# Kernel optimization log

Measured on AMD Instinct MI355X. Metric: run time of the kernel, lower is better.

Reference implementation:

```python
import jax, jax.numpy as jnp
import numpy as np

N, H, W_SP, CIN = 32, 56, 56, 256
COUT, KH, KW = 256, 3, 3


def setup_inputs() -> dict:
    key = jax.random.key(0)
    k1, k2, k3 = jax.random.split(key, 3)
    x = jax.random.normal(k1, (N, H, W_SP, CIN), dtype=jnp.float32)
    W = jax.random.normal(k2, (KH, KW, CIN, COUT), dtype=jnp.float32) * 0.05
    b = jax.random.normal(k3, (COUT,), dtype=jnp.float32) * 0.05
    return {"x": x, "W": W, "b": b}


def reference(x, W, b):
    # Binarize weights to {-1, +1} via sign with straight-through estimator
    # (forward = sign(W), gradient = identity), matching tensorlayer's
    # binary_weight quantizer.
    bW = W + jax.lax.stop_gradient(jnp.sign(W) - W)
    # tf.nn.conv2d(x, bW, strides=(1,1,1,1), padding='SAME'), NHWC / HWIO
    y = jax.lax.conv_general_dilated(
        x, bW,
        window_strides=(1, 1),
        padding='SAME',
        dimension_numbers=('NHWC', 'HWIO', 'NHWC'),
    )
    y = y + b  # tf.nn.bias_add over channels
    return jax.nn.relu(y)
```

## Files before the change

### kernel.cpp

```cpp
#include <hip/hip_runtime.h>
#include <hip/hip_bf16.h>

#define CIN   256
#define COUT  256
#define HH    56
#define WW    56
#define NB    32
#define KTOT  2304
#define MTOT  (NB * HH * WW)

#define BM 128
#define BN 256
#define BK 32
#define NTHREADS 256
#define NSTEPS (KTOT / BK)

#define BT_BYTES  ((size_t)COUT * KTOT * 2)
#define XB_OFF    BT_BYTES
#define XB_BYTES  ((size_t)MTOT * CIN * 2)
#define ZB_OFF    (XB_OFF + XB_BYTES)
#define WS_NEEDED (ZB_OFF + 64)

typedef __attribute__((ext_vector_type(4))) float  f32x4;
typedef __attribute__((ext_vector_type(8))) __bf16 bf16x8;

__device__ __forceinline__ void gload_lds16(const void* g, void* l) {
    __builtin_amdgcn_global_load_lds(
        (const __attribute__((address_space(1))) void*)g,
        (__attribute__((address_space(3))) void*)l,
        16, 0, 0);
}

__global__ void xcast_kernel(const float* __restrict__ x, __bf16* __restrict__ xb,
                             float* __restrict__ zbuf) {
    const size_t total = (size_t)MTOT * CIN / 8;
    size_t idx = (size_t)blockIdx.x * blockDim.x + threadIdx.x;
    const size_t stride = (size_t)gridDim.x * blockDim.x;
    for (size_t g = idx; g < total; g += stride) {
        f32x4 v0 = ((const f32x4*)x)[2 * g];
        f32x4 v1 = ((const f32x4*)x)[2 * g + 1];
        bf16x8 o;
        o[0] = (__bf16)v0[0]; o[1] = (__bf16)v0[1];
        o[2] = (__bf16)v0[2]; o[3] = (__bf16)v0[3];
        o[4] = (__bf16)v1[0]; o[5] = (__bf16)v1[1];
        o[6] = (__bf16)v1[2]; o[7] = (__bf16)v1[3];
        ((bf16x8*)xb)[g] = o;
    }
    if (blockIdx.x == 0 && threadIdx.x < 16) zbuf[threadIdx.x] = 0.f;
}

__global__ void binarize_w_kernel(const float* __restrict__ W,
                                  unsigned short* __restrict__ bt) {
    int k  = blockIdx.x;
    int co = threadIdx.x;
    int tap = k >> 8, cin = k & 255;
    int c2 = cin >> 5, ci = cin & 31;
    int ks = c2 * 9 + tap;
    float w = W[(size_t)k * COUT + co];
    unsigned short s = (w > 0.f) ? 0x3F80u : ((w < 0.f) ? 0xBF80u : 0u);
    bt[(size_t)co * KTOT + ks * 32 + (ci ^ (((co >> 1) & 3) << 3))] = s;
}

__global__ __launch_bounds__(NTHREADS, 2)
void bconv_kernel(const __bf16* __restrict__ xb,
                  const unsigned short* __restrict__ bt,
                  const float* __restrict__ bias,
                  float* __restrict__ out,
                  const char* __restrict__ zb) {
    __shared__ __bf16 Al[2][BM][BK];
    __shared__ __bf16 Bl[2][BN][BK];

    const int tid  = threadIdx.x;
    const int lane = tid & 63;
    const int wid  = tid >> 6;

    const int bid = blockIdx.x;
    const int swz = (bid & 7) * (MTOT / BM / 8) + (bid >> 3);
    const int m_base = swz * BM;

    const int wn = wid * 64;

    long bBase[4];
#pragma unroll
    for (int j = 0; j < 4; ++j) {
        int co = j * 64 + wid * 16 + (lane >> 2);
        bBase[j] = (long)co * (KTOT * 2) + (long)(lane & 3) * 16;
    }

    const int schunk = (lane & 3) ^ ((lane >> 3) & 3);
    int aH[2], aW[2];
    long aBase[2];
#pragma unroll
    for (int i = 0; i < 2; ++i) {
        int r = wid * 32 + i * 16 + (lane >> 2);
        int flat = m_base + r;
        aW[i] = flat % WW;
        aH[i] = (flat / WW) % HH;
        aBase[i] = (long)flat * (CIN * 2) + schunk * 16;
    }

    f32x4 acc[8][4];
#pragma unroll
    for (int i = 0; i < 8; ++i)
#pragma unroll
        for (int j = 0; j < 4; ++j)
            acc[i][j] = (f32x4){0.f, 0.f, 0.f, 0.f};

    const char* xbb = (const char*)xb;
    const char* btb = (const char*)bt;

    auto STAGE = [&](int ks, int buf) {
#pragma unroll
        for (int j = 0; j < 4; ++j)
            gload_lds16(btb + bBase[j] + (long)ks * 64,
                        &Bl[buf][j * 64 + wid * 16][0]);
        const int c2  = ks / 9;
        const int tap = ks - c2 * 9;
        const int dh  = tap / 3 - 1;
        const int dw  = tap % 3 - 1;
        const long doff = (long)(dh * WW + dw) * (CIN * 2);
#pragma unroll
        for (int i = 0; i < 2; ++i) {
            int ih = aH[i] + dh, iw = aW[i] + dw;
            bool valid = ((unsigned)ih < (unsigned)HH) && ((unsigned)iw < (unsigned)WW);
            const char* g = valid ? (xbb + aBase[i] + doff + c2 * 64)
                                  : (const char*)zb;
            gload_lds16(g, &Al[buf][wid * 32 + i * 16][0]);
        }
    };

    STAGE(0, 0);

    const int rsel = lane & 15;
    const int cbyte = ((lane >> 4) ^ ((rsel >> 1) & 3)) * 16;

    for (int ks = 0; ks < NSTEPS; ++ks) {
        const int cur = ks & 1;
        if (ks + 1 < NSTEPS) {
            STAGE(ks + 1, cur ^ 1);
            asm volatile("s_waitcnt vmcnt(6)" ::: "memory");
        } else {
            asm volatile("s_waitcnt vmcnt(0)" ::: "memory");
        }
        __builtin_amdgcn_s_barrier();
        asm volatile("" ::: "memory");

        const char* Ab = (const char*)&Al[cur][0][0];
        const char* Bb = (const char*)&Bl[cur][0][0];
        bf16x8 af[8], bfr[4];
#pragma unroll
        for (int ni = 0; ni < 4; ++ni)
            bfr[ni] = *(const bf16x8*)(Bb + (wn + ni * 16 + rsel) * (BK * 2) + cbyte);
#pragma unroll
        for (int mi = 0; mi < 8; ++mi)
            af[mi] = *(const bf16x8*)(Ab + (mi * 16 + rsel) * (BK * 2) + cbyte);

        __builtin_amdgcn_s_setprio(1);
#pragma unroll
        for (int mi = 0; mi < 8; ++mi)
#pragma unroll
            for (int ni = 0; ni < 4; ++ni)
                acc[mi][ni] = __builtin_amdgcn_mfma_f32_16x16x32_bf16(
                    af[mi], bfr[ni], acc[mi][ni], 0, 0, 0);
        __builtin_amdgcn_s_setprio(0);

        asm volatile("s_waitcnt lgkmcnt(0)" ::: "memory");
        __builtin_amdgcn_s_barrier();
        asm volatile("" ::: "memory");
    }

    const int col_l  = lane & 15;
    const int row_g4 = (lane >> 4) * 4;
#pragma unroll
    for (int ni = 0; ni < 4; ++ni) {
        const int cout = wn + ni * 16 + col_l;
        const float bv = bias[cout];
#pragma unroll
        for (int mi = 0; mi < 8; ++mi) {
            const int row = m_base + mi * 16 + row_g4;
#pragma unroll
            for (int j = 0; j < 4; ++j) {
                float v = acc[mi][ni][j] + bv;
                out[(size_t)(row + j) * COUT + cout] = v > 0.f ? v : 0.f;
            }
        }
    }
}

__global__ void binarize_w_old_kernel(const float* __restrict__ W,
                                      unsigned short* __restrict__ bt) {
    int k  = blockIdx.x;
    int co = threadIdx.x;
    int tap = k >> 8, cin = k & 255;
    int c = cin >> 6, ci = cin & 63;
    int ks = c * 9 + tap;
    float w = W[(size_t)k * COUT + co];
    unsigned short s = (w > 0.f) ? 0x3F80u : ((w < 0.f) ? 0xBF80u : 0u);
    bt[(size_t)co * KTOT + ks * 64 + (ci ^ ((co & 7) << 3))] = s;
}

__global__ __launch_bounds__(512, 4)
void bconv_old_kernel(const float* __restrict__ x,
                      const unsigned short* __restrict__ bt,
                      const float* __restrict__ bias,
                      float* __restrict__ out) {
    __shared__ __bf16 Al[128][64];
    __shared__ __bf16 Bl[256][64];

    const int tid  = threadIdx.x;
    const int lane = tid & 63;
    const int wid  = tid >> 6;

    const int bid = blockIdx.x;
    const int swz = (bid & 7) * (MTOT / 128 / 8) + (bid >> 3);
    const int m_base = swz * 128;

    const int wm = (wid & 1) * 64;
    const int wn = (wid >> 1) * 64;

    const int  rB0 = wid * 32 + (lane >> 3);
    const long bB0 = (long)rB0 * (KTOT * 2) + (lane & 7) * 16;

    int aH[2], aW[2], aOff[2];
#pragma unroll
    for (int i = 0; i < 2; ++i) {
        int r = i * 64 + (tid >> 3);
        int flat = m_base + r;
        aW[i] = flat % WW;
        aH[i] = (flat / WW) % HH;
        aOff[i] = flat * (CIN * 4);
    }

    f32x4 acc[4][4];
#pragma unroll
    for (int i = 0; i < 4; ++i)
#pragma unroll
        for (int j = 0; j < 4; ++j)
            acc[i][j] = (f32x4){0.f, 0.f, 0.f, 0.f};

    const char* xfb = (const char*)x;
    const char* btb = (const char*)bt;

    for (int ks = 0; ks < 36; ++ks) {
        const int c    = ks / 9;
        const int tap  = ks % 9;
        const int dh   = tap / 3 - 1;
        const int dw   = tap % 3 - 1;
        const int doff = dh * WW + dw;

        __syncthreads();

#pragma unroll
        for (int i = 0; i < 4; ++i) {
            const char* g = btb + bB0 + (long)i * 8 * (KTOT * 2) + ks * 128;
            gload_lds16(g, &Bl[wid * 32 + i * 8][0]);
        }

        const int cg = tid & 7;
#pragma unroll
        for (int i = 0; i < 2; ++i) {
            int ih = aH[i] + dh, iw = aW[i] + dw;
            f32x4 v0 = (f32x4){0.f, 0.f, 0.f, 0.f};
            f32x4 v1 = (f32x4){0.f, 0.f, 0.f, 0.f};
            if (((unsigned)ih < (unsigned)HH) && ((unsigned)iw < (unsigned)WW)) {
                const float* gp = (const float*)(xfb +
                    (long)(aOff[i] + doff * (CIN * 4) + c * 256 + cg * 32));
                v0 = ((const f32x4*)gp)[0];
                v1 = ((const f32x4*)gp)[1];
            }
            bf16x8 o;
            o[0] = (__bf16)v0[0]; o[1] = (__bf16)v0[1];
            o[2] = (__bf16)v0[2]; o[3] = (__bf16)v0[3];
            o[4] = (__bf16)v1[0]; o[5] = (__bf16)v1[1];
            o[6] = (__bf16)v1[2]; o[7] = (__bf16)v1[3];
            int r = i * 64 + (tid >> 3);
            *(bf16x8*)((char*)&Al[0][0] + r * 128 + ((cg * 16) ^ ((r & 7) << 4))) = o;
        }

        __syncthreads();

        const char* Ab = (const char*)&Al[0][0];
        const char* Bb = (const char*)&Bl[0][0];
        const int swzr = (lane & 7) << 4;
        const int rsel = lane & 15;
        const int csel = (lane >> 4) * 16;
#pragma unroll
        for (int kk = 0; kk < 2; ++kk) {
            const int colb = kk * 64 + csel;
            bf16x8 af[4], bfr[4];
#pragma unroll
            for (int mi = 0; mi < 4; ++mi)
                af[mi] = *(const bf16x8*)(Ab + (wm + mi * 16 + rsel) * 128 + (colb ^ swzr));
#pragma unroll
            for (int ni = 0; ni < 4; ++ni)
                bfr[ni] = *(const bf16x8*)(Bb + (wn + ni * 16 + rsel) * 128 + (colb ^ swzr));
#pragma unroll
            for (int mi = 0; mi < 4; ++mi)
#pragma unroll
                for (int ni = 0; ni < 4; ++ni)
                    acc[mi][ni] = __builtin_amdgcn_mfma_f32_16x16x32_bf16(
                        af[mi], bfr[ni], acc[mi][ni], 0, 0, 0);
        }
    }

    const int col_l  = lane & 15;
    const int row_g4 = (lane >> 4) * 4;
#pragma unroll
    for (int ni = 0; ni < 4; ++ni) {
        const int cout = wn + ni * 16 + col_l;
        const float bv = bias[cout];
#pragma unroll
        for (int mi = 0; mi < 4; ++mi) {
            const int row = m_base + wm + mi * 16 + row_g4;
#pragma unroll
            for (int j = 0; j < 4; ++j) {
                float v = acc[mi][ni][j] + bv;
                out[(size_t)(row + j) * COUT + cout] = v > 0.f ? v : 0.f;
            }
        }
    }
}

extern "C" void kernel_launch(void* const* d_in, const int* in_sizes, int n_in,
                              void* d_out, int out_size, void* d_ws, size_t ws_size,
                              hipStream_t stream) {
    const float* x = (const float*)d_in[0];
    const float* W = (const float*)d_in[1];
    const float* b = (const float*)d_in[2];
    float* out = (float*)d_out;

    char* ws = (char*)d_ws;
    unsigned short* bt = (unsigned short*)ws;
    __bf16* xb   = (__bf16*)(ws + XB_OFF);
    float*  zbuf = (float*)(ws + ZB_OFF);

    if (ws_size >= WS_NEEDED) {
        binarize_w_kernel<<<dim3(KTOT), dim3(COUT), 0, stream>>>(W, bt);
        xcast_kernel<<<dim3(2048), dim3(256), 0, stream>>>(x, xb, zbuf);
        bconv_kernel<<<dim3(MTOT / BM), dim3(NTHREADS), 0, stream>>>(
            xb, bt, b, out, (const char*)zbuf);
    } else {
        binarize_w_old_kernel<<<dim3(KTOT), dim3(COUT), 0, stream>>>(W, bt);
        bconv_old_kernel<<<dim3(MTOT / 128), dim3(512), 0, stream>>>(x, bt, b, out);
    }
}
```

Measured before the change: 182.4 us.

## Use 8-wave blocks with 2x4 warp tiling and triple-buffered LDS prefetch

The block grows from 4 to 8 waves arranged as a 2x4 grid, so each wave computes a 64x64 sub-tile instead of 128x64. This halves per-wave accumulators and fragment loads, and each thread issues fewer global-to-LDS loads per stage. The single double buffer becomes a three-slot LDS ring that prefetches two K-steps ahead, with vmcnt waits adjusted to match, to hide more global load latency. The new launch bound of 4 blocks of 512 threads may squeeze the register budget and cause spills, and the larger LDS footprint limits how many blocks fit on a CU.

```diff
diff --git a/kernel.cpp b/kernel.cpp
--- a/kernel.cpp
+++ b/kernel.cpp
@@ -12,8 +12,9 @@
 #define BM 128
 #define BN 256
 #define BK 32
-#define NTHREADS 256
+#define NTHREADS 512
 #define NSTEPS (KTOT / BK)
+#define SLOT_ELEMS (BM * BK + BN * BK)
 
 #define BT_BYTES  ((size_t)COUT * KTOT * 2)
 #define XB_OFF    BT_BYTES
@@ -61,14 +62,13 @@
     bt[(size_t)co * KTOT + ks * 32 + (ci ^ (((co >> 1) & 3) << 3))] = s;
 }
 
-__global__ __launch_bounds__(NTHREADS, 2)
+__global__ __launch_bounds__(NTHREADS, 4)
 void bconv_kernel(const __bf16* __restrict__ xb,
                   const unsigned short* __restrict__ bt,
                   const float* __restrict__ bias,
                   float* __restrict__ out,
                   const char* __restrict__ zb) {
-    __shared__ __bf16 Al[2][BM][BK];
-    __shared__ __bf16 Bl[2][BN][BK];
+    __shared__ __bf16 lds[3 * SLOT_ELEMS];
 
     const int tid  = threadIdx.x;
     const int lane = tid & 63;
@@ -78,30 +78,30 @@
     const int swz = (bid & 7) * (MTOT / BM / 8) + (bid >> 3);
     const int m_base = swz * BM;
 
-    const int wn = wid * 64;
-
-    long bBase[4];
-#pragma unroll
-    for (int j = 0; j < 4; ++j) {
-        int co = j * 64 + wid * 16 + (lane >> 2);
-        bBase[j] = (long)co * (KTOT * 2) + (long)(lane & 3) * 16;
-    }
-
-    const int schunk = (lane & 3) ^ ((lane >> 3) & 3);
-    int aH[2], aW[2];
-    long aBase[2];
-#pragma unroll
-    for (int i = 0; i < 2; ++i) {
-        int r = wid * 32 + i * 16 + (lane >> 2);
+    const int wm = (wid >> 2) * 64;
+    const int wn = (wid & 3) * 64;
+
+    long bSrc[2];
+#pragma unroll
+    for (int j = 0; j < 2; ++j) {
+        int co = j * 128 + (tid >> 2);
+        bSrc[j] = (long)co * (KTOT * 2) + (long)(tid & 3) * 16;
+    }
+
+    const int schunk = (tid & 3) ^ ((tid >> 3) & 3);
+    int aHH, aWW;
+    long aBase;
+    {
+        int r = tid >> 2;
         int flat = m_base + r;
-        aW[i] = flat % WW;
-        aH[i] = (flat / WW) % HH;
-        aBase[i] = (long)flat * (CIN * 2) + schunk * 16;
-    }
-
-    f32x4 acc[8][4];
-#pragma unroll
-    for (int i = 0; i < 8; ++i)
+        aWW = flat % WW;
+        aHH = (flat / WW) % HH;
+        aBase = (long)flat * (CIN * 2) + schunk * 16;
+    }
+
+    f32x4 acc[4][4];
+#pragma unroll
+    for (int i = 0; i < 4; ++i)
 #pragma unroll
         for (int j = 0; j < 4; ++j)
             acc[i][j] = (f32x4){0.f, 0.f, 0.f, 0.f};
@@ -109,55 +109,59 @@
     const char* xbb = (const char*)xb;
     const char* btb = (const char*)bt;
 
-    auto STAGE = [&](int ks, int buf) {
-#pragma unroll
-        for (int j = 0; j < 4; ++j)
-            gload_lds16(btb + bBase[j] + (long)ks * 64,
-                        &Bl[buf][j * 64 + wid * 16][0]);
+    auto STAGE = [&](int ks, int slot) {
+        __bf16* As = &lds[slot * SLOT_ELEMS];
+        __bf16* Bs = As + BM * BK;
+#pragma unroll
+        for (int j = 0; j < 2; ++j)
+            gload_lds16(btb + bSrc[j] + (long)ks * 64,
+                        &Bs[(j * 128 + wid * 16) * BK]);
         const int c2  = ks / 9;
         const int tap = ks - c2 * 9;
         const int dh  = tap / 3 - 1;
         const int dw  = tap % 3 - 1;
-        const long doff = (long)(dh * WW + dw) * (CIN * 2);
-#pragma unroll
-        for (int i = 0; i < 2; ++i) {
-            int ih = aH[i] + dh, iw = aW[i] + dw;
-            bool valid = ((unsigned)ih < (unsigned)HH) && ((unsigned)iw < (unsigned)WW);
-            const char* g = valid ? (xbb + aBase[i] + doff + c2 * 64)
-                                  : (const char*)zb;
-            gload_lds16(g, &Al[buf][wid * 32 + i * 16][0]);
-        }
+        int ih = aHH + dh, iw = aWW + dw;
+        bool valid = ((unsigned)ih < (unsigned)HH) && ((unsigned)iw < (unsigned)WW);
+        const char* g = valid
+            ? (xbb + aBase + (long)(dh * WW + dw) * (CIN * 2) + c2 * 64)
+            : (const char*)zb;
+        gload_lds16(g, &As[(wid * 16) * BK]);
     };
 
     STAGE(0, 0);
-
-    const int rsel = lane & 15;
+    STAGE(1, 1);
+
+    const int rsel  = lane & 15;
     const int cbyte = ((lane >> 4) ^ ((rsel >> 1) & 3)) * 16;
 
-    for (int ks = 0; ks < NSTEPS; ++ks) {
-        const int cur = ks & 1;
-        if (ks + 1 < NSTEPS) {
-            STAGE(ks + 1, cur ^ 1);
+    int sc = 0;
+    for (int t = 0; t < NSTEPS; ++t) {
+        if (t < NSTEPS - 2) {
+            const int sp = (sc >= 1) ? (sc - 1) : 2;
+            STAGE(t + 2, sp);
             asm volatile("s_waitcnt vmcnt(6)" ::: "memory");
+        } else if (t == NSTEPS - 2) {
+            asm volatile("s_waitcnt vmcnt(3)" ::: "memory");
         } else {
             asm volatile("s_waitcnt vmcnt(0)" ::: "memory");
         }
         __builtin_amdgcn_s_barrier();
         asm volatile("" ::: "memory");
 
-        const char* Ab = (const char*)&Al[cur][0][0];
-        const char* Bb = (const char*)&Bl[cur][0][0];
-        bf16x8 af[8], bfr[4];
+        const char* As = (const char*)&lds[sc * SLOT_ELEMS];
+        const char* Bs = As + BM * BK * 2;
+
+        bf16x8 af[4], bfr[4];
+#pragma unroll
+        for (int mi = 0; mi < 4; ++mi)
+            af[mi] = *(const bf16x8*)(As + (wm + mi * 16 + rsel) * (BK * 2) + cbyte);
 #pragma unroll
         for (int ni = 0; ni < 4; ++ni)
-            bfr[ni] = *(const bf16x8*)(Bb + (wn + ni * 16 + rsel) * (BK * 2) + cbyte);
-#pragma unroll
-        for (int mi = 0; mi < 8; ++mi)
-            af[mi] = *(const bf16x8*)(Ab + (mi * 16 + rsel) * (BK * 2) + cbyte);
+            bfr[ni] = *(const bf16x8*)(Bs + (wn + ni * 16 + rsel) * (BK * 2) + cbyte);
 
         __builtin_amdgcn_s_setprio(1);
 #pragma unroll
-        for (int mi = 0; mi < 8; ++mi)
+        for (int mi = 0; mi < 4; ++mi)
 #pragma unroll
             for (int ni = 0; ni < 4; ++ni)
                 acc[mi][ni] = __builtin_amdgcn_mfma_f32_16x16x32_bf16(
@@ -167,6 +171,8 @@
         asm volatile("s_waitcnt lgkmcnt(0)" ::: "memory");
         __builtin_amdgcn_s_barrier();
         asm volatile("" ::: "memory");
+
+        sc = (sc < 2) ? (sc + 1) : 0;
     }
 
     const int col_l  = lane & 15;
@@ -176,8 +182,8 @@
         const int cout = wn + ni * 16 + col_l;
         const float bv = bias[cout];
 #pragma unroll
-        for (int mi = 0; mi < 8; ++mi) {
-            const int row = m_base + mi * 16 + row_g4;
+        for (int mi = 0; mi < 4; ++mi) {
+            const int row = m_base + wm + mi * 16 + row_g4;
 #pragma unroll
             for (int j = 0; j < 4; ++j) {
                 float v = acc[mi][ni][j] + bv;
```

Measured after the change: 157.5 us. 13.6% less time.

## Retile bconv to 256x128 blocks with 2x2 warp grid and N split

Applied to the files above, without the earlier changes.

Changes the block tile from 128x256 (M x N) to 256x128. The grid now splits the output channels in two, and the 4 waves are arranged as a 2x2 grid with 128x64 per-wave tiles. A unified LDS buffer replaces the separate A/B arrays, and launch bounds are raised to 3 blocks per CU to increase occupancy. The x tile is now fetched once per N-half, which doubles activation traffic. In exchange the grid is doubled and occupancy is higher, while the per-wave MFMA work and LDS footprint stay the same.

```diff
diff --git a/kernel.cpp b/kernel.cpp
--- a/kernel.cpp
+++ b/kernel.cpp
@@ -9,11 +9,12 @@
 #define KTOT  2304
 #define MTOT  (NB * HH * WW)
 
-#define BM 128
-#define BN 256
+#define BM 256
+#define BN 128
 #define BK 32
 #define NTHREADS 256
 #define NSTEPS (KTOT / BK)
+#define SLOT_ELEMS ((BM + BN) * BK)
 
 #define BT_BYTES  ((size_t)COUT * KTOT * 2)
 #define XB_OFF    BT_BYTES
@@ -61,38 +62,39 @@
     bt[(size_t)co * KTOT + ks * 32 + (ci ^ (((co >> 1) & 3) << 3))] = s;
 }
 
-__global__ __launch_bounds__(NTHREADS, 2)
+__global__ __launch_bounds__(NTHREADS, 3)
 void bconv_kernel(const __bf16* __restrict__ xb,
                   const unsigned short* __restrict__ bt,
                   const float* __restrict__ bias,
                   float* __restrict__ out,
                   const char* __restrict__ zb) {
-    __shared__ __bf16 Al[2][BM][BK];
-    __shared__ __bf16 Bl[2][BN][BK];
+    __shared__ __bf16 lds[2 * SLOT_ELEMS];
 
     const int tid  = threadIdx.x;
     const int lane = tid & 63;
     const int wid  = tid >> 6;
 
     const int bid = blockIdx.x;
-    const int swz = (bid & 7) * (MTOT / BM / 8) + (bid >> 3);
-    const int m_base = swz * BM;
-
-    const int wn = wid * 64;
-
-    long bBase[4];
-#pragma unroll
-    for (int j = 0; j < 4; ++j) {
-        int co = j * 64 + wid * 16 + (lane >> 2);
-        bBase[j] = (long)co * (KTOT * 2) + (long)(lane & 3) * 16;
-    }
-
-    const int schunk = (lane & 3) ^ ((lane >> 3) & 3);
-    int aH[2], aW[2];
-    long aBase[2];
-#pragma unroll
-    for (int i = 0; i < 2; ++i) {
-        int r = wid * 32 + i * 16 + (lane >> 2);
+    const int swz = (bid & 7) * 98 + (bid >> 3);
+    const int m_base = (swz >> 1) * BM;
+    const int n_base = (swz & 1) * BN;
+
+    const int wm = (wid >> 1) * 128;
+    const int wn = (wid & 1) * 64;
+
+    long bSrc[2];
+#pragma unroll
+    for (int j = 0; j < 2; ++j) {
+        int co = n_base + j * 64 + (tid >> 2);
+        bSrc[j] = (long)co * (KTOT * 2) + (long)(tid & 3) * 16;
+    }
+
+    const int schunk = (tid & 3) ^ ((tid >> 3) & 3);
+    int aH[4], aW[4];
+    long aBase[4];
+#pragma unroll
+    for (int i = 0; i < 4; ++i) {
+        int r = i * 64 + (tid >> 2);
         int flat = m_base + r;
         aW[i] = flat % WW;
         aH[i] = (flat / WW) % HH;
@@ -109,35 +111,36 @@
     const char* xbb = (const char*)xb;
     const char* btb = (const char*)bt;
 
-    auto STAGE = [&](int ks, int buf) {
-#pragma unroll
-        for (int j = 0; j < 4; ++j)
-            gload_lds16(btb + bBase[j] + (long)ks * 64,
-                        &Bl[buf][j * 64 + wid * 16][0]);
+    auto STAGE = [&](int ks, int slot) {
+        __bf16* As = &lds[slot * SLOT_ELEMS];
+        __bf16* Bs = As + BM * BK;
+#pragma unroll
+        for (int j = 0; j < 2; ++j)
+            gload_lds16(btb + bSrc[j] + (long)ks * 64,
+                        &Bs[(j * 64 + wid * 16) * BK]);
         const int c2  = ks / 9;
         const int tap = ks - c2 * 9;
         const int dh  = tap / 3 - 1;
         const int dw  = tap % 3 - 1;
-        const long doff = (long)(dh * WW + dw) * (CIN * 2);
-#pragma unroll
-        for (int i = 0; i < 2; ++i) {
+        const long soff = (long)(dh * WW + dw) * (CIN * 2) + c2 * 64;
+#pragma unroll
+        for (int i = 0; i < 4; ++i) {
             int ih = aH[i] + dh, iw = aW[i] + dw;
             bool valid = ((unsigned)ih < (unsigned)HH) && ((unsigned)iw < (unsigned)WW);
-            const char* g = valid ? (xbb + aBase[i] + doff + c2 * 64)
-                                  : (const char*)zb;
-            gload_lds16(g, &Al[buf][wid * 32 + i * 16][0]);
+            const char* g = valid ? (xbb + aBase[i] + soff) : (const char*)zb;
+            gload_lds16(g, &As[(i * 64 + wid * 16) * BK]);
         }
     };
 
     STAGE(0, 0);
 
-    const int rsel = lane & 15;
+    const int rsel  = lane & 15;
     const int cbyte = ((lane >> 4) ^ ((rsel >> 1) & 3)) * 16;
 
-    for (int ks = 0; ks < NSTEPS; ++ks) {
-        const int cur = ks & 1;
-        if (ks + 1 < NSTEPS) {
-            STAGE(ks + 1, cur ^ 1);
+    for (int t = 0; t < NSTEPS; ++t) {
+        const int cur = t & 1;
+        if (t + 1 < NSTEPS) {
+            STAGE(t + 1, cur ^ 1);
             asm volatile("s_waitcnt vmcnt(6)" ::: "memory");
         } else {
             asm volatile("s_waitcnt vmcnt(0)" ::: "memory");
@@ -145,15 +148,16 @@
         __builtin_amdgcn_s_barrier();
         asm volatile("" ::: "memory");
 
-        const char* Ab = (const char*)&Al[cur][0][0];
-        const char* Bb = (const char*)&Bl[cur][0][0];
+        const char* As = (const char*)&lds[cur * SLOT_ELEMS];
+        const char* Bs = As + BM * BK * 2;
+
         bf16x8 af[8], bfr[4];
 #pragma unroll
         for (int ni = 0; ni < 4; ++ni)
-            bfr[ni] = *(const bf16x8*)(Bb + (wn + ni * 16 + rsel) * (BK * 2) + cbyte);
+            bfr[ni] = *(const bf16x8*)(Bs + (wn + ni * 16 + rsel) * (BK * 2) + cbyte);
 #pragma unroll
         for (int mi = 0; mi < 8; ++mi)
-            af[mi] = *(const bf16x8*)(Ab + (mi * 16 + rsel) * (BK * 2) + cbyte);
+            af[mi] = *(const bf16x8*)(As + (wm + mi * 16 + rsel) * (BK * 2) + cbyte);
 
         __builtin_amdgcn_s_setprio(1);
 #pragma unroll
@@ -173,11 +177,11 @@
     const int row_g4 = (lane >> 4) * 4;
 #pragma unroll
     for (int ni = 0; ni < 4; ++ni) {
-        const int cout = wn + ni * 16 + col_l;
+        const int cout = n_base + wn + ni * 16 + col_l;
         const float bv = bias[cout];
 #pragma unroll
         for (int mi = 0; mi < 8; ++mi) {
-            const int row = m_base + mi * 16 + row_g4;
+            const int row = m_base + wm + mi * 16 + row_g4;
 #pragma unroll
             for (int j = 0; j < 4; ++j) {
                 float v = acc[mi][ni][j] + bv;
@@ -337,7 +341,7 @@
     if (ws_size >= WS_NEEDED) {
         binarize_w_kernel<<<dim3(KTOT), dim3(COUT), 0, stream>>>(W, bt);
         xcast_kernel<<<dim3(2048), dim3(256), 0, stream>>>(x, xb, zbuf);
-        bconv_kernel<<<dim3(MTOT / BM), dim3(NTHREADS), 0, stream>>>(
+        bconv_kernel<<<dim3((MTOT / BM) * (COUT / BN)), dim3(NTHREADS), 0, stream>>>(
             xb, bt, b, out, (const char*)zbuf);
     } else {
         binarize_w_old_kernel<<<dim3(KTOT), dim3(COUT), 0, stream>>>(W, bt);
```

After: 680.8 us. +273.3%, slower.

## Enlarge conv GEMM tile to 256x256 with split-K-half interleaved LDS pipeline

Applied to the files above, without the earlier changes.

Doubles the M tile to 256 rows and the thread count to 512, arranging 8 waves as a 2x4 grid. Each 64-wide K step is split into two 32-wide halves held in separate LDS regions, and the global-to-LDS loads for the next halves are issued between MFMA phases. This raises operand reuse per LDS byte and hides load latency under compute. The cost is a 128KB LDS footprint, which allows only one block per CU, and a grid with a partial last wave of blocks.

```diff
diff --git a/kernel.cpp b/kernel.cpp
--- a/kernel.cpp
+++ b/kernel.cpp
@@ -9,11 +9,11 @@
 #define KTOT  2304
 #define MTOT  (NB * HH * WW)
 
-#define BM 128
+#define BM 256
 #define BN 256
-#define BK 32
-#define NTHREADS 256
-#define NSTEPS (KTOT / BK)
+#define NTHREADS 512
+#define NT 36
+#define REG_ELEMS (256 * 32)
 
 #define BT_BYTES  ((size_t)COUT * KTOT * 2)
 #define XB_OFF    BT_BYTES
@@ -67,37 +67,34 @@
                   const float* __restrict__ bias,
                   float* __restrict__ out,
                   const char* __restrict__ zb) {
-    __shared__ __bf16 Al[2][BM][BK];
-    __shared__ __bf16 Bl[2][BN][BK];
+    __shared__ __bf16 lds[2][4][REG_ELEMS];
 
     const int tid  = threadIdx.x;
     const int lane = tid & 63;
     const int wid  = tid >> 6;
 
     const int bid = blockIdx.x;
-    const int swz = (bid & 7) * (MTOT / BM / 8) + (bid >> 3);
+    const int swz = (bid & 7) * 49 + (bid >> 3);
     const int m_base = swz * BM;
 
-    const int wn = wid * 64;
-
-    long bBase[4];
-#pragma unroll
-    for (int j = 0; j < 4; ++j) {
-        int co = j * 64 + wid * 16 + (lane >> 2);
-        bBase[j] = (long)co * (KTOT * 2) + (long)(lane & 3) * 16;
-    }
-
-    const int schunk = (lane & 3) ^ ((lane >> 3) & 3);
+    const int wm = (wid >> 2) * 128;
+    const int wn = (wid & 3) * 64;
+
+    const int schunk = (tid & 3) ^ ((tid >> 3) & 3);
     int aH[2], aW[2];
     long aBase[2];
 #pragma unroll
-    for (int i = 0; i < 2; ++i) {
-        int r = wid * 32 + i * 16 + (lane >> 2);
+    for (int j = 0; j < 2; ++j) {
+        int r = j * 128 + (tid >> 2);
         int flat = m_base + r;
-        aW[i] = flat % WW;
-        aH[i] = (flat / WW) % HH;
-        aBase[i] = (long)flat * (CIN * 2) + schunk * 16;
-    }
+        aW[j] = flat % WW;
+        aH[j] = (flat / WW) % HH;
+        aBase[j] = (long)flat * (CIN * 2) + schunk * 16;
+    }
+    long bBase[2];
+#pragma unroll
+    for (int j = 0; j < 2; ++j)
+        bBase[j] = (long)(j * 128 + (tid >> 2)) * (KTOT * 2) + (long)(tid & 3) * 16;
 
     f32x4 acc[8][4];
 #pragma unroll
@@ -109,64 +106,84 @@
     const char* xbb = (const char*)xb;
     const char* btb = (const char*)bt;
 
-    auto STAGE = [&](int ks, int buf) {
-#pragma unroll
-        for (int j = 0; j < 4; ++j)
-            gload_lds16(btb + bBase[j] + (long)ks * 64,
-                        &Bl[buf][j * 64 + wid * 16][0]);
-        const int c2  = ks / 9;
-        const int tap = ks - c2 * 9;
+    auto STAGE_A = [&](int ks, int h, int buf) {
+        const int c   = ks / 9;
+        const int tap = ks - c * 9;
         const int dh  = tap / 3 - 1;
         const int dw  = tap % 3 - 1;
-        const long doff = (long)(dh * WW + dw) * (CIN * 2);
-#pragma unroll
-        for (int i = 0; i < 2; ++i) {
-            int ih = aH[i] + dh, iw = aW[i] + dw;
+        const long soff = (long)(dh * WW + dw) * (CIN * 2) + c * 128 + h * 64;
+#pragma unroll
+        for (int j = 0; j < 2; ++j) {
+            int ih = aH[j] + dh, iw = aW[j] + dw;
             bool valid = ((unsigned)ih < (unsigned)HH) && ((unsigned)iw < (unsigned)WW);
-            const char* g = valid ? (xbb + aBase[i] + doff + c2 * 64)
-                                  : (const char*)zb;
-            gload_lds16(g, &Al[buf][wid * 32 + i * 16][0]);
+            const char* g = valid ? (xbb + aBase[j] + soff) : (const char*)zb;
+            gload_lds16(g, (char*)&lds[buf][h][0] + j * 8192 + wid * 1024);
         }
     };
-
-    STAGE(0, 0);
-
-    const int rsel = lane & 15;
+    auto STAGE_B = [&](int ks, int h, int buf) {
+        const int c   = ks / 9;
+        const int tap = ks - c * 9;
+        const long soff = (long)(((2 * c + h) * 9 + tap)) * 64;
+#pragma unroll
+        for (int j = 0; j < 2; ++j)
+            gload_lds16(btb + bBase[j] + soff,
+                        (char*)&lds[buf][2 + h][0] + j * 8192 + wid * 1024);
+    };
+
+    STAGE_A(0, 0, 0); STAGE_B(0, 0, 0);
+    STAGE_A(0, 1, 0); STAGE_B(0, 1, 0);
+    STAGE_A(1, 0, 1); STAGE_B(1, 0, 1);
+
+    const int rsel  = lane & 15;
     const int cbyte = ((lane >> 4) ^ ((rsel >> 1) & 3)) * 16;
 
-    for (int ks = 0; ks < NSTEPS; ++ks) {
-        const int cur = ks & 1;
-        if (ks + 1 < NSTEPS) {
-            STAGE(ks + 1, cur ^ 1);
-            asm volatile("s_waitcnt vmcnt(6)" ::: "memory");
-        } else {
-            asm volatile("s_waitcnt vmcnt(0)" ::: "memory");
-        }
+    bf16x8 bfr[4];
+    auto PH = [&](const char* Ar, const char* Br, int mf0, bool readB) {
+        if (readB) {
+#pragma unroll
+            for (int ni = 0; ni < 4; ++ni)
+                bfr[ni] = *(const bf16x8*)(Br + (wn + ni * 16 + rsel) * 64 + cbyte);
+        }
+        bf16x8 af[4];
+#pragma unroll
+        for (int k = 0; k < 4; ++k)
+            af[k] = *(const bf16x8*)(Ar + (wm + (mf0 + k) * 16 + rsel) * 64 + cbyte);
+        __builtin_amdgcn_s_setprio(1);
+#pragma unroll
+        for (int k = 0; k < 4; ++k)
+#pragma unroll
+            for (int ni = 0; ni < 4; ++ni)
+                acc[mf0 + k][ni] = __builtin_amdgcn_mfma_f32_16x16x32_bf16(
+                    af[k], bfr[ni], acc[mf0 + k][ni], 0, 0, 0);
+        __builtin_amdgcn_s_setprio(0);
+    };
+
+    for (int t = 0; t < NT; ++t) {
+        const int cur = t & 1;
+        if (t == NT - 1) { asm volatile("s_waitcnt vmcnt(4)" ::: "memory"); }
+        else             { asm volatile("s_waitcnt vmcnt(8)" ::: "memory"); }
         __builtin_amdgcn_s_barrier();
         asm volatile("" ::: "memory");
 
-        const char* Ab = (const char*)&Al[cur][0][0];
-        const char* Bb = (const char*)&Bl[cur][0][0];
-        bf16x8 af[8], bfr[4];
-#pragma unroll
-        for (int ni = 0; ni < 4; ++ni)
-            bfr[ni] = *(const bf16x8*)(Bb + (wn + ni * 16 + rsel) * (BK * 2) + cbyte);
-#pragma unroll
-        for (int mi = 0; mi < 8; ++mi)
-            af[mi] = *(const bf16x8*)(Ab + (mi * 16 + rsel) * (BK * 2) + cbyte);
-
-        __builtin_amdgcn_s_setprio(1);
-#pragma unroll
-        for (int mi = 0; mi < 8; ++mi)
-#pragma unroll
-            for (int ni = 0; ni < 4; ++ni)
-                acc[mi][ni] = __builtin_amdgcn_mfma_f32_16x16x32_bf16(
-                    af[mi], bfr[ni], acc[mi][ni], 0, 0, 0);
-        __builtin_amdgcn_s_setprio(0);
-
-        asm volatile("s_waitcnt lgkmcnt(0)" ::: "memory");
+        const char* A0r = (const char*)&lds[cur][0][0];
+        const char* A1r = (const char*)&lds[cur][1][0];
+        const char* B0r = (const char*)&lds[cur][2][0];
+        const char* B1r = (const char*)&lds[cur][3][0];
+
+        if (t + 1 < NT) STAGE_A(t + 1, 1, cur ^ 1);
+        PH(A0r, B0r, 0, true);
+        if (t + 1 < NT) STAGE_B(t + 1, 1, cur ^ 1);
+        PH(A0r, B0r, 4, false);
+
+        if (t == NT - 1) { asm volatile("s_waitcnt vmcnt(0)" ::: "memory"); }
+        else             { asm volatile("s_waitcnt vmcnt(8)" ::: "memory"); }
         __builtin_amdgcn_s_barrier();
         asm volatile("" ::: "memory");
+
+        if (t + 2 < NT) STAGE_A(t + 2, 0, cur);
+        PH(A1r, B1r, 0, true);
+        if (t + 2 < NT) STAGE_B(t + 2, 0, cur);
+        PH(A1r, B1r, 4, false);
     }
 
     const int col_l  = lane & 15;
@@ -177,7 +194,7 @@
         const float bv = bias[cout];
 #pragma unroll
         for (int mi = 0; mi < 8; ++mi) {
-            const int row = m_base + mi * 16 + row_g4;
+            const int row = m_base + wm + mi * 16 + row_g4;
 #pragma unroll
             for (int j = 0; j < 4; ++j) {
                 float v = acc[mi][ni][j] + bv;
```

Result: faster. 163.6 us (-10.3%).
